# Kernel tuning notes

Measured on AMD Instinct MI355X. Metric: run time of the kernel, lower is better.

The kernel has to match this reference:

```python
import jax, jax.numpy as jnp
import numpy as np
import math

B, T, C = 2, 2048, 1024
H = 16
D = C // H


def setup_inputs() -> dict:
    key = jax.random.key(0)
    ks = jax.random.split(key, 5)
    s = 1.0 / math.sqrt(C)
    return {
        "x": jax.random.normal(ks[0], (B, T, C), dtype=jnp.float32),
        "W_qkv": jax.random.normal(ks[1], (C, 3 * C), dtype=jnp.float32) * s,
        "b_qkv": jnp.zeros((3 * C,), dtype=jnp.float32),
        "W_proj": jax.random.normal(ks[2], (C, C), dtype=jnp.float32) * s,
        "b_proj": jnp.zeros((C,), dtype=jnp.float32),
    }


def reference(x, W_qkv, b_qkv, W_proj, b_proj):
    qkv = x @ W_qkv + b_qkv  # [B,T,3C]
    q, k, v = jnp.split(qkv, 3, axis=-1)
    # [B,T,C] -> [B,H,T,D]
    q = q.reshape(B, T, H, D).transpose(0, 2, 1, 3)
    k = k.reshape(B, T, H, D).transpose(0, 2, 1, 3)
    v = v.reshape(B, T, H, D).transpose(0, 2, 1, 3)
    sm_scale = 1.0 / math.sqrt(D)
    att = jnp.einsum("bhqd,bhkd->bhqk", q, k) * sm_scale
    causal = jnp.tril(jnp.ones((T, T), dtype=bool))  # True = keep
    att = jnp.where(causal, att, -jnp.inf)
    att = jax.nn.softmax(att, axis=-1)
    y = jnp.einsum("bhqk,bhkd->bhqd", att, v)  # [B,H,T,D]
    y = y.transpose(0, 2, 1, 3).reshape(B, T, C)
    return y @ W_proj + b_proj
```

## Files before the change

kernel.cpp:

```cpp
#include <hip/hip_runtime.h>
#include <hip/hip_bf16.h>
#include <math.h>

#define BB 2
#define TT 2048
#define CCH 1024
#define HH 16
#define DD 64
#define BT (BB*TT)
#define N3 (3*CCH)
#define NJOBS 40

typedef __attribute__((ext_vector_type(8))) short short8;
typedef __attribute__((ext_vector_type(4))) float f32x4;
typedef __attribute__((ext_vector_type(16))) float f32x16;

__device__ __forceinline__ unsigned short f2bf(float f) {
  unsigned int u = __float_as_uint(f);
  unsigned int r = (u + 0x7FFFu + ((u >> 16) & 1u)) >> 16;
  return (unsigned short)r;
}
__device__ __forceinline__ float bf2f(unsigned short u) {
  return __uint_as_float(((unsigned int)u) << 16);
}
__device__ __forceinline__ int cvtpk(float lo, float hi) {
  int r;
  asm("v_cvt_pk_bf16_f32 %0, %1, %2" : "=v"(r) : "v"(lo), "v"(hi));
  return r;
}
__device__ __forceinline__ void plswap(int &a, int &b) {
  asm("v_permlane32_swap_b32 %0, %1" : "+v"(a), "+v"(b));
}
__device__ __forceinline__ float fexp2(float x) {
  float r;
  asm("v_exp_f32 %0, %1" : "=v"(r) : "v"(x));
  return r;
}
__device__ __forceinline__ void gload_lds16(const unsigned short* g, unsigned short* l) {
  __builtin_amdgcn_global_load_lds((const __attribute__((address_space(1))) void*)g,
                                   (__attribute__((address_space(3))) void*)l, 16, 0, 0);
}
__device__ __forceinline__ float fmax3(float a, float b, float c) {
  return fmaxf(fmaxf(a, b), c);
}
__device__ __forceinline__ int jbase(int qt) {
  int a = qt >> 2, b = qt & 3;
  return qt + 2 * a * (a - 1) + a * b;
}

__global__ __launch_bounds__(256) void k_convert(const float* __restrict__ in,
                                                 unsigned short* __restrict__ out, int n8) {
  int i = blockIdx.x * 256 + threadIdx.x;
  if (i < n8) {
    const float4 a = *(const float4*)(in + (size_t)i * 8);
    const float4 b = *(const float4*)(in + (size_t)i * 8 + 4);
    short8 v;
    v[0] = f2bf(a.x); v[1] = f2bf(a.y); v[2] = f2bf(a.z); v[3] = f2bf(a.w);
    v[4] = f2bf(b.x); v[5] = f2bf(b.y); v[6] = f2bf(b.z); v[7] = f2bf(b.w);
    *(short8*)(out + (size_t)i * 8) = v;
  }
}

__global__ __launch_bounds__(256) void k_transpose_cvt(const float* __restrict__ in,
                                                       unsigned short* __restrict__ out,
                                                       int R, int Cn) {
  __shared__ float tile[32][33];
  int tc = blockIdx.x * 32;
  int tr = blockIdx.y * 32;
  int lx = threadIdx.x & 31;
  int ly = threadIdx.x >> 5;
#pragma unroll
  for (int i = 0; i < 32; i += 8)
    tile[ly + i][lx] = in[(size_t)(tr + ly + i) * Cn + tc + lx];
  __syncthreads();
#pragma unroll
  for (int i = 0; i < 32; i += 8)
    out[(size_t)(tc + ly + i) * R + tr + lx] = f2bf(tile[lx][ly + i]);
}

__global__ __launch_bounds__(256) void k_qkv_gemm(const unsigned short* __restrict__ Xb,
                                                  const unsigned short* __restrict__ Wt,
                                                  const float* __restrict__ bias,
                                                  unsigned short* __restrict__ Qo,
                                                  unsigned short* __restrict__ Ko,
                                                  unsigned short* __restrict__ Vto) {
  __shared__ __align__(16) unsigned short As[128 * 32];
  __shared__ __align__(16) unsigned short Bs[128 * 32];
  int tid = threadIdx.x;
  int mb = blockIdx.x * 128;
  int nb = blockIdx.y * 128;
  int wid = tid >> 6, lane = tid & 63;
  int wr = (wid >> 1) * 64, wc = (wid & 1) * 64;
  int l15 = lane & 15, l4 = lane >> 4;
  int l16 = lane >> 2, lc = (lane & 3) * 8;
  f32x4 acc[4][4];
#pragma unroll
  for (int a = 0; a < 4; ++a)
#pragma unroll
    for (int b = 0; b < 4; ++b)
#pragma unroll
      for (int j = 0; j < 4; ++j) acc[a][b][j] = 0.0f;

  for (int kb = 0; kb < CCH; kb += 32) {
#pragma unroll
    for (int i = 0; i < 2; ++i) {
      int arow = wid * 32 + i * 16;
      gload_lds16(Xb + (size_t)(mb + arow + l16) * CCH + kb + lc, &As[arow * 32]);
      gload_lds16(Wt + (size_t)(nb + arow + l16) * CCH + kb + lc, &Bs[arow * 32]);
    }
    __syncthreads();
    short8 af[4], bfr[4];
#pragma unroll
    for (int mt = 0; mt < 4; ++mt) af[mt] = *(const short8*)(&As[(wr + mt * 16 + l15) * 32 + l4 * 8]);
#pragma unroll
    for (int nt = 0; nt < 4; ++nt) bfr[nt] = *(const short8*)(&Bs[(wc + nt * 16 + l15) * 32 + l4 * 8]);
#pragma unroll
    for (int mt = 0; mt < 4; ++mt)
#pragma unroll
      for (int nt = 0; nt < 4; ++nt)
        acc[mt][nt] = __builtin_amdgcn_mfma_f32_16x16x32_bf16(af[mt], bfr[nt], acc[mt][nt], 0, 0, 0);
    __syncthreads();
  }

#pragma unroll
  for (int mt = 0; mt < 4; ++mt) {
#pragma unroll
    for (int nt = 0; nt < 4; ++nt) {
      int gcol = nb + wc + nt * 16 + l15;
      int which = gcol >> 10;
      int cc = gcol & 1023;
      int h = cc >> 6, d = cc & 63;
      float bv = bias[gcol];
#pragma unroll
      for (int j = 0; j < 4; ++j) {
        int grow = mb + wr + mt * 16 + l4 * 4 + j;
        int b = grow >> 11, t = grow & 2047;
        float v = acc[mt][nt][j] + bv;
        size_t bh = (size_t)(b * HH + h);
        if (which == 0)      Qo[(bh * TT + t) * DD + d] = f2bf(v * 0.18033688f);
        else if (which == 1) Ko[(bh * TT + t) * DD + d] = f2bf(v);
        else                 Vto[(bh * DD + d) * TT + t] = f2bf(v);
      }
    }
  }
}

__global__ __launch_bounds__(256) void k_attn(const unsigned short* __restrict__ Qb,
                                              const unsigned short* __restrict__ Kb,
                                              const unsigned short* __restrict__ Vtb,
                                              unsigned short* __restrict__ PO,
                                              float* __restrict__ Pm,
                                              float* __restrict__ Pl) {
  __shared__ unsigned short Ks[2][64 * 64];
  __shared__ unsigned short Vs[2][64 * 64];
  int tid = threadIdx.x;
  int jx = blockIdx.x;
  int bh = blockIdx.y;
  int qt = 0;
#pragma unroll
  for (int q = 1; q < 16; ++q)
    if (jx >= jbase(q)) qt = q;
  int chunk = jx - jbase(qt);
  int t0 = chunk * 8;
  int t1 = min(t0 + 8, (qt + 1) * 2);
  size_t job = (size_t)bh * NJOBS + jx;

  const unsigned short* Qp = Qb + (size_t)bh * TT * DD;
  const unsigned short* Kp = Kb + (size_t)bh * TT * DD;
  const unsigned short* Vp = Vtb + (size_t)bh * DD * TT;
  int wid = tid >> 6, lane = tid & 63;
  int l31 = lane & 31, h = lane >> 5;
  int q0 = qt * 128 + wid * 32;
  int qrow = q0 + l31;

  short8 qf[4];
#pragma unroll
  for (int m = 0; m < 4; ++m)
    qf[m] = *(const short8*)(Qp + (size_t)qrow * DD + m * 16 + h * 8);

  f32x16 zv;
#pragma unroll
  for (int r = 0; r < 16; ++r) zv[r] = 0.0f;

  f32x16 po[2];
  po[0] = zv; po[1] = zv;
  float mrun = -1e30f, lrun = 0.0f;

  short8 rk[2], rv[2];
#pragma unroll
  for (int i = 0; i < 2; ++i) {
    int idx = tid + i * 256;
    int row = idx >> 3, c = idx & 7;
    rk[i] = *(const short8*)(Kp + (size_t)(t0 * 64 + row) * DD + c * 8);
    rv[i] = *(const short8*)(Vp + (size_t)row * TT + t0 * 64 + c * 8);
  }
#pragma unroll
  for (int i = 0; i < 2; ++i) {
    int idx = tid + i * 256;
    int row = idx >> 3, c = idx & 7;
    int off = row * 64 + ((c ^ (row & 7)) * 8);
    *(short8*)(&Ks[0][off]) = rk[i];
    *(short8*)(&Vs[0][off]) = rv[i];
  }

  int buf = 0;
  for (int t = t0; t < t1; ++t) {
    __syncthreads();
    int kvb = t * 64;
    bool havenext = (t + 1 < t1);
    if (havenext) {
      int kvb2 = (t + 1) * 64;
#pragma unroll
      for (int i = 0; i < 2; ++i) {
        int idx = tid + i * 256;
        int row = idx >> 3, c = idx & 7;
        rk[i] = *(const short8*)(Kp + (size_t)(kvb2 + row) * DD + c * 8);
        rv[i] = *(const short8*)(Vp + (size_t)row * TT + kvb2 + c * 8);
      }
    }

    if (kvb <= q0 + 31) {
      f32x16 st[2];
      __builtin_amdgcn_s_setprio(1);
#pragma unroll
      for (int t32 = 0; t32 < 2; ++t32) {
        int row = t32 * 32 + l31;
        {
          int off = row * 64 + ((h ^ (row & 7)) * 8);
          short8 kf = *(const short8*)(&Ks[buf][off]);
          st[t32] = __builtin_amdgcn_mfma_f32_32x32x16_bf16(kf, qf[0], zv, 0, 0, 0);
        }
#pragma unroll
        for (int m = 1; m < 4; ++m) {
          int off = row * 64 + (((2 * m + h) ^ (row & 7)) * 8);
          short8 kf = *(const short8*)(&Ks[buf][off]);
          st[t32] = __builtin_amdgcn_mfma_f32_32x32x16_bf16(kf, qf[m], st[t32], 0, 0, 0);
        }
      }
      __builtin_amdgcn_s_setprio(0);

      if (kvb + 63 > q0) {
#pragma unroll
        for (int t32 = 0; t32 < 2; ++t32)
#pragma unroll
          for (int r = 0; r < 16; ++r) {
            int kvg = kvb + t32 * 32 + (r & 3) + 8 * (r >> 2) + 4 * h;
            if (kvg > qrow) st[t32][r] = -1e30f;
          }
      }

      float A = st[0][0], B = st[0][1], C = st[0][2], Dv = st[0][3];
#pragma unroll
      for (int r = 4; r < 16; r += 4) {
        A = fmax3(A, st[0][r], st[0][r + 1]);
        B = fmax3(B, st[0][r + 2], st[0][r + 3]);
        C = fmax3(C, st[1][r - 4], st[1][r - 3]);
        Dv = fmax3(Dv, st[1][r - 2], st[1][r - 1]);
      }
      C = fmax3(C, st[1][12], st[1][13]);
      Dv = fmax3(Dv, st[1][14], st[1][15]);
      float mx = fmaxf(fmax3(A, B, C), Dv);
      mx = fmaxf(mx, __shfl_xor(mx, 32));

      if (__any(mx - mrun > 8.0f)) {
        float mnew = fmaxf(mrun, mx);
        float alpha = fexp2(mrun - mnew);
        lrun *= alpha;
#pragma unroll
        for (int dt = 0; dt < 2; ++dt)
#pragma unroll
          for (int r = 0; r < 16; ++r) po[dt][r] *= alpha;
        mrun = mnew;
      }

      float sum = 0.0f;
#pragma unroll
      for (int t32 = 0; t32 < 2; ++t32)
#pragma unroll
        for (int r = 0; r < 16; ++r) {
          float p = fexp2(st[t32][r] - mrun);
          st[t32][r] = p;
          sum += p;
        }
      sum += __shfl_xor(sum, 32);
      lrun += sum;

      short8 pf[4];
#pragma unroll
      for (int g = 0; g < 4; ++g) {
        int t32 = g >> 1, r0 = (g & 1) * 8;
        int a = cvtpk(st[t32][r0 + 0], st[t32][r0 + 1]);
        int b = cvtpk(st[t32][r0 + 4], st[t32][r0 + 5]);
        plswap(a, b);
        int c = cvtpk(st[t32][r0 + 2], st[t32][r0 + 3]);
        int d = cvtpk(st[t32][r0 + 6], st[t32][r0 + 7]);
        plswap(c, d);
        union { int w[4]; short8 s; } u;
        u.w[0] = a; u.w[1] = c; u.w[2] = b; u.w[3] = d;
        pf[g] = u.s;
      }

      __builtin_amdgcn_s_setprio(1);
#pragma unroll
      for (int dt = 0; dt < 2; ++dt) {
#pragma unroll
        for (int g = 0; g < 4; ++g) {
          int row = dt * 32 + l31;
          int off = row * 64 + (((2 * g + h) ^ (row & 7)) * 8);
          short8 vf = *(const short8*)(&Vs[buf][off]);
          po[dt] = __builtin_amdgcn_mfma_f32_32x32x16_bf16(vf, pf[g], po[dt], 0, 0, 0);
        }
      }
      __builtin_amdgcn_s_setprio(0);
    }

    if (havenext) {
#pragma unroll
      for (int i = 0; i < 2; ++i) {
        int idx = tid + i * 256;
        int row = idx >> 3, c = idx & 7;
        int off = row * 64 + ((c ^ (row & 7)) * 8);
        *(short8*)(&Ks[buf ^ 1][off]) = rk[i];
        *(short8*)(&Vs[buf ^ 1][off]) = rv[i];
      }
    }
    buf ^= 1;
  }

  int wrow = wid * 32 + l31;
  size_t pobase = (job * 128 + wrow) * 64;
#pragma unroll
  for (int dt = 0; dt < 2; ++dt)
#pragma unroll
    for (int r = 0; r < 16; r += 2) {
      int d = dt * 32 + (r & 3) + 8 * (r >> 2) + 4 * h;
      int w = cvtpk(po[dt][r], po[dt][r + 1]);
      *(int*)(PO + pobase + d) = w;
    }
  if (h == 0) {
    Pm[job * 128 + wrow] = mrun;
    Pl[job * 128 + wrow] = lrun;
  }
}

__global__ __launch_bounds__(256) void k_attn_combine(const unsigned short* __restrict__ PO,
                                                      const float* __restrict__ Pm,
                                                      const float* __restrict__ Pl,
                                                      unsigned short* __restrict__ Y) {
  int qt = blockIdx.x, bh = blockIdx.y;
  int nc = (qt >> 2) + 1;
  size_t job0 = (size_t)bh * NJOBS + jbase(qt);
  int tid = threadIdx.x;
  int row = tid >> 1, half = tid & 1;

  float m[4], l[4];
  float M = -1e30f;
  for (int c = 0; c < nc; ++c) {
    m[c] = Pm[(job0 + c) * 128 + row];
    l[c] = Pl[(job0 + c) * 128 + row];
    M = fmaxf(M, m[c]);
  }
  float L = 0.0f, w[4];
  for (int c = 0; c < nc; ++c) {
    w[c] = fexp2(m[c] - M);
    L += l[c] * w[c];
  }
  float inv = 1.0f / L;

  float acc[32];
#pragma unroll
  for (int j = 0; j < 32; ++j) acc[j] = 0.0f;
  for (int c = 0; c < nc; ++c) {
    const unsigned short* p = PO + ((job0 + c) * 128 + row) * 64 + half * 32;
    float wc = w[c];
#pragma unroll
    for (int k = 0; k < 4; ++k) {
      short8 v = *(const short8*)(p + k * 8);
#pragma unroll
      for (int j = 0; j < 8; ++j) acc[k * 8 + j] += wc * bf2f((unsigned short)v[j]);
    }
  }
  int b = bh >> 4, hh = bh & 15;
  int t = qt * 128 + row;
  unsigned short* yp = Y + ((size_t)(b * TT + t)) * CCH + hh * DD + half * 32;
#pragma unroll
  for (int k = 0; k < 4; ++k) {
    short8 wv;
#pragma unroll
    for (int j = 0; j < 8; ++j) wv[j] = (short)f2bf(acc[k * 8 + j] * inv);
    *(short8*)(yp + k * 8) = wv;
  }
}

__global__ __launch_bounds__(256) void k_proj_gemm(const unsigned short* __restrict__ Yb,
                                                   const unsigned short* __restrict__ Wt,
                                                   const float* __restrict__ bias,
                                                   float* __restrict__ Out) {
  __shared__ __align__(16) unsigned short As[128 * 32];
  __shared__ __align__(16) unsigned short Bs[128 * 32];
  int tid = threadIdx.x;
  int mb = blockIdx.x * 128;
  int nb = blockIdx.y * 128;
  int wid = tid >> 6, lane = tid & 63;
  int wr = (wid >> 1) * 64, wc = (wid & 1) * 64;
  int l15 = lane & 15, l4 = lane >> 4;
  int l16 = lane >> 2, lc = (lane & 3) * 8;
  f32x4 acc[4][4];
#pragma unroll
  for (int a = 0; a < 4; ++a)
#pragma unroll
    for (int b = 0; b < 4; ++b)
#pragma unroll
      for (int j = 0; j < 4; ++j) acc[a][b][j] = 0.0f;

  for (int kb = 0; kb < CCH; kb += 32) {
#pragma unroll
    for (int i = 0; i < 2; ++i) {
      int arow = wid * 32 + i * 16;
      gload_lds16(Yb + (size_t)(mb + arow + l16) * CCH + kb + lc, &As[arow * 32]);
      gload_lds16(Wt + (size_t)(nb + arow + l16) * CCH + kb + lc, &Bs[arow * 32]);
    }
    __syncthreads();
    short8 af[4], bfr[4];
#pragma unroll
    for (int mt = 0; mt < 4; ++mt) af[mt] = *(const short8*)(&As[(wr + mt * 16 + l15) * 32 + l4 * 8]);
#pragma unroll
    for (int nt = 0; nt < 4; ++nt) bfr[nt] = *(const short8*)(&Bs[(wc + nt * 16 + l15) * 32 + l4 * 8]);
#pragma unroll
    for (int mt = 0; mt < 4; ++mt)
#pragma unroll
      for (int nt = 0; nt < 4; ++nt)
        acc[mt][nt] = __builtin_amdgcn_mfma_f32_16x16x32_bf16(af[mt], bfr[nt], acc[mt][nt], 0, 0, 0);
    __syncthreads();
  }

#pragma unroll
  for (int mt = 0; mt < 4; ++mt) {
#pragma unroll
    for (int nt = 0; nt < 4; ++nt) {
      int gcol = nb + wc + nt * 16 + l15;
      float bv = bias[gcol];
#pragma unroll
      for (int j = 0; j < 4; ++j) {
        int grow = mb + wr + mt * 16 + l4 * 4 + j;
        Out[(size_t)grow * CCH + gcol] = acc[mt][nt][j] + bv;
      }
    }
  }
}

extern "C" void kernel_launch(void* const* d_in, const int* in_sizes, int n_in,
                              void* d_out, int out_size, void* d_ws, size_t ws_size,
                              hipStream_t stream) {
  const float* x      = (const float*)d_in[0];
  const float* W_qkv  = (const float*)d_in[1];
  const float* b_qkv  = (const float*)d_in[2];
  const float* W_proj = (const float*)d_in[3];
  const float* b_proj = (const float*)d_in[4];
  float* out = (float*)d_out;

  char* ws = (char*)d_ws;
  size_t off = 0;
  unsigned short* Wt_qkv  = (unsigned short*)(ws + off); off += (size_t)N3 * CCH * 2;
  unsigned short* Wt_proj = (unsigned short*)(ws + off); off += (size_t)CCH * CCH * 2;
  unsigned short* Xb      = (unsigned short*)(ws + off); off += (size_t)BT * CCH * 2;
  unsigned short* Qb      = (unsigned short*)(ws + off); off += (size_t)BT * CCH * 2;
  unsigned short* Kb      = (unsigned short*)(ws + off); off += (size_t)BT * CCH * 2;
  unsigned short* Vt      = (unsigned short*)(ws + off); off += (size_t)BT * CCH * 2;
  unsigned short* Yb      = (unsigned short*)(ws + off); off += (size_t)BT * CCH * 2;
  unsigned short* PO      = (unsigned short*)(ws + off); off += (size_t)32 * NJOBS * 128 * 64 * 2;
  float*          Pm      = (float*)(ws + off);          off += (size_t)32 * NJOBS * 128 * 4;
  float*          Pl      = (float*)(ws + off);          off += (size_t)32 * NJOBS * 128 * 4;

  k_convert<<<dim3(BT * CCH / 8 / 256), 256, 0, stream>>>(x, Xb, BT * CCH / 8);
  k_transpose_cvt<<<dim3(N3 / 32, CCH / 32), 256, 0, stream>>>(W_qkv, Wt_qkv, CCH, N3);
  k_transpose_cvt<<<dim3(CCH / 32, CCH / 32), 256, 0, stream>>>(W_proj, Wt_proj, CCH, CCH);
  k_qkv_gemm<<<dim3(BT / 128, N3 / 128), 256, 0, stream>>>(Xb, Wt_qkv, b_qkv, Qb, Kb, Vt);
  k_attn<<<dim3(NJOBS, BB * HH), 256, 0, stream>>>(Qb, Kb, Vt, PO, Pm, Pl);
  k_attn_combine<<<dim3(TT / 128, BB * HH), 256, 0, stream>>>(PO, Pm, Pl, Yb);
  k_proj_gemm<<<dim3(BT / 128, CCH / 128), 256, 0, stream>>>(Yb, Wt_proj, b_proj, out);
}
```

Baseline: 130.2 us.

## Read K/V fragments directly from global memory instead of LDS double buffer

Removes the shared-memory double-buffered K/V staging and the per-iteration barrier from the attention kernel. Each wave now loads its MFMA K and V operand fragments straight from global memory, relying on L1/L2 caching for reuse across the four waves, and exits the loop early once past the causal limit. This drops the LDS traffic and the sync, and frees LDS for higher occupancy. In exchange each wave issues redundant global loads with no explicit prefetch, so load latency lands directly on the MFMA chain.

```diff
diff --git a/kernel.cpp b/kernel.cpp
--- a/kernel.cpp
+++ b/kernel.cpp
@@ -151,8 +151,6 @@
                                               unsigned short* __restrict__ PO,
                                               float* __restrict__ Pm,
                                               float* __restrict__ Pl) {
-  __shared__ unsigned short Ks[2][64 * 64];
-  __shared__ unsigned short Vs[2][64 * 64];
   int tid = threadIdx.x;
   int jx = blockIdx.x;
   int bh = blockIdx.y;
@@ -186,145 +184,94 @@
   po[0] = zv; po[1] = zv;
   float mrun = -1e30f, lrun = 0.0f;
 
-  short8 rk[2], rv[2];
-#pragma unroll
-  for (int i = 0; i < 2; ++i) {
-    int idx = tid + i * 256;
-    int row = idx >> 3, c = idx & 7;
-    rk[i] = *(const short8*)(Kp + (size_t)(t0 * 64 + row) * DD + c * 8);
-    rv[i] = *(const short8*)(Vp + (size_t)row * TT + t0 * 64 + c * 8);
-  }
-#pragma unroll
-  for (int i = 0; i < 2; ++i) {
-    int idx = tid + i * 256;
-    int row = idx >> 3, c = idx & 7;
-    int off = row * 64 + ((c ^ (row & 7)) * 8);
-    *(short8*)(&Ks[0][off]) = rk[i];
-    *(short8*)(&Vs[0][off]) = rv[i];
-  }
-
-  int buf = 0;
   for (int t = t0; t < t1; ++t) {
-    __syncthreads();
     int kvb = t * 64;
-    bool havenext = (t + 1 < t1);
-    if (havenext) {
-      int kvb2 = (t + 1) * 64;
-#pragma unroll
-      for (int i = 0; i < 2; ++i) {
-        int idx = tid + i * 256;
-        int row = idx >> 3, c = idx & 7;
-        rk[i] = *(const short8*)(Kp + (size_t)(kvb2 + row) * DD + c * 8);
-        rv[i] = *(const short8*)(Vp + (size_t)row * TT + kvb2 + c * 8);
+    if (kvb > q0 + 31) break;
+
+    f32x16 st[2];
+    __builtin_amdgcn_s_setprio(1);
+#pragma unroll
+    for (int t32 = 0; t32 < 2; ++t32) {
+      const unsigned short* kbase = Kp + (size_t)(kvb + t32 * 32 + l31) * DD + h * 8;
+      st[t32] = __builtin_amdgcn_mfma_f32_32x32x16_bf16(*(const short8*)kbase, qf[0], zv, 0, 0, 0);
+#pragma unroll
+      for (int m = 1; m < 4; ++m)
+        st[t32] = __builtin_amdgcn_mfma_f32_32x32x16_bf16(*(const short8*)(kbase + m * 16), qf[m],
+                                                          st[t32], 0, 0, 0);
+    }
+    __builtin_amdgcn_s_setprio(0);
+
+    if (kvb + 63 > q0) {
+#pragma unroll
+      for (int t32 = 0; t32 < 2; ++t32)
+#pragma unroll
+        for (int r = 0; r < 16; ++r) {
+          int kvg = kvb + t32 * 32 + (r & 3) + 8 * (r >> 2) + 4 * h;
+          if (kvg > qrow) st[t32][r] = -1e30f;
+        }
+    }
+
+    float A = st[0][0], B = st[0][1], C = st[0][2], Dv = st[0][3];
+#pragma unroll
+    for (int r = 4; r < 16; r += 4) {
+      A = fmax3(A, st[0][r], st[0][r + 1]);
+      B = fmax3(B, st[0][r + 2], st[0][r + 3]);
+      C = fmax3(C, st[1][r - 4], st[1][r - 3]);
+      Dv = fmax3(Dv, st[1][r - 2], st[1][r - 1]);
+    }
+    C = fmax3(C, st[1][12], st[1][13]);
+    Dv = fmax3(Dv, st[1][14], st[1][15]);
+    float mx = fmaxf(fmax3(A, B, C), Dv);
+    mx = fmaxf(mx, __shfl_xor(mx, 32));
+
+    if (__any(mx - mrun > 8.0f)) {
+      float mnew = fmaxf(mrun, mx);
+      float alpha = fexp2(mrun - mnew);
+      lrun *= alpha;
+#pragma unroll
+      for (int dt = 0; dt < 2; ++dt)
+#pragma unroll
+        for (int r = 0; r < 16; ++r) po[dt][r] *= alpha;
+      mrun = mnew;
+    }
+
+    float sum = 0.0f;
+#pragma unroll
+    for (int t32 = 0; t32 < 2; ++t32)
+#pragma unroll
+      for (int r = 0; r < 16; ++r) {
+        float p = fexp2(st[t32][r] - mrun);
+        st[t32][r] = p;
+        sum += p;
       }
-    }
-
-    if (kvb <= q0 + 31) {
-      f32x16 st[2];
-      __builtin_amdgcn_s_setprio(1);
-#pragma unroll
-      for (int t32 = 0; t32 < 2; ++t32) {
-        int row = t32 * 32 + l31;
-        {
-          int off = row * 64 + ((h ^ (row & 7)) * 8);
-          short8 kf = *(const short8*)(&Ks[buf][off]);
-          st[t32] = __builtin_amdgcn_mfma_f32_32x32x16_bf16(kf, qf[0], zv, 0, 0, 0);
-        }
-#pragma unroll
-        for (int m = 1; m < 4; ++m) {
-          int off = row * 64 + (((2 * m + h) ^ (row & 7)) * 8);
-          short8 kf = *(const short8*)(&Ks[buf][off]);
-          st[t32] = __builtin_amdgcn_mfma_f32_32x32x16_bf16(kf, qf[m], st[t32], 0, 0, 0);
-        }
-      }
-      __builtin_amdgcn_s_setprio(0);
-
-      if (kvb + 63 > q0) {
-#pragma unroll
-        for (int t32 = 0; t32 < 2; ++t32)
-#pragma unroll
-          for (int r = 0; r < 16; ++r) {
-            int kvg = kvb + t32 * 32 + (r & 3) + 8 * (r >> 2) + 4 * h;
-            if (kvg > qrow) st[t32][r] = -1e30f;
-          }
-      }
-
-      float A = st[0][0], B = st[0][1], C = st[0][2], Dv = st[0][3];
-#pragma unroll
-      for (int r = 4; r < 16; r += 4) {
-        A = fmax3(A, st[0][r], st[0][r + 1]);
-        B = fmax3(B, st[0][r + 2], st[0][r + 3]);
-        C = fmax3(C, st[1][r - 4], st[1][r - 3]);
-        Dv = fmax3(Dv, st[1][r - 2], st[1][r - 1]);
-      }
-      C = fmax3(C, st[1][12], st[1][13]);
-      Dv = fmax3(Dv, st[1][14], st[1][15]);
-      float mx = fmaxf(fmax3(A, B, C), Dv);
-      mx = fmaxf(mx, __shfl_xor(mx, 32));
-
-      if (__any(mx - mrun > 8.0f)) {
-        float mnew = fmaxf(mrun, mx);
-        float alpha = fexp2(mrun - mnew);
-        lrun *= alpha;
-#pragma unroll
-        for (int dt = 0; dt < 2; ++dt)
-#pragma unroll
-          for (int r = 0; r < 16; ++r) po[dt][r] *= alpha;
-        mrun = mnew;
-      }
-
-      float sum = 0.0f;
-#pragma unroll
-      for (int t32 = 0; t32 < 2; ++t32)
-#pragma unroll
-        for (int r = 0; r < 16; ++r) {
-          float p = fexp2(st[t32][r] - mrun);
-          st[t32][r] = p;
-          sum += p;
-        }
-      sum += __shfl_xor(sum, 32);
-      lrun += sum;
-
-      short8 pf[4];
-#pragma unroll
-      for (int g = 0; g < 4; ++g) {
-        int t32 = g >> 1, r0 = (g & 1) * 8;
-        int a = cvtpk(st[t32][r0 + 0], st[t32][r0 + 1]);
-        int b = cvtpk(st[t32][r0 + 4], st[t32][r0 + 5]);
-        plswap(a, b);
-        int c = cvtpk(st[t32][r0 + 2], st[t32][r0 + 3]);
-        int d = cvtpk(st[t32][r0 + 6], st[t32][r0 + 7]);
-        plswap(c, d);
-        union { int w[4]; short8 s; } u;
-        u.w[0] = a; u.w[1] = c; u.w[2] = b; u.w[3] = d;
-        pf[g] = u.s;
-      }
-
-      __builtin_amdgcn_s_setprio(1);
-#pragma unroll
-      for (int dt = 0; dt < 2; ++dt) {
-#pragma unroll
-        for (int g = 0; g < 4; ++g) {
-          int row = dt * 32 + l31;
-          int off = row * 64 + (((2 * g + h) ^ (row & 7)) * 8);
-          short8 vf = *(const short8*)(&Vs[buf][off]);
-          po[dt] = __builtin_amdgcn_mfma_f32_32x32x16_bf16(vf, pf[g], po[dt], 0, 0, 0);
-        }
-      }
-      __builtin_amdgcn_s_setprio(0);
-    }
-
-    if (havenext) {
-#pragma unroll
-      for (int i = 0; i < 2; ++i) {
-        int idx = tid + i * 256;
-        int row = idx >> 3, c = idx & 7;
-        int off = row * 64 + ((c ^ (row & 7)) * 8);
-        *(short8*)(&Ks[buf ^ 1][off]) = rk[i];
-        *(short8*)(&Vs[buf ^ 1][off]) = rv[i];
-      }
-    }
-    buf ^= 1;
+    sum += __shfl_xor(sum, 32);
+    lrun += sum;
+
+    short8 pf[4];
+#pragma unroll
+    for (int g = 0; g < 4; ++g) {
+      int t32 = g >> 1, r0 = (g & 1) * 8;
+      int a = cvtpk(st[t32][r0 + 0], st[t32][r0 + 1]);
+      int b = cvtpk(st[t32][r0 + 4], st[t32][r0 + 5]);
+      plswap(a, b);
+      int c = cvtpk(st[t32][r0 + 2], st[t32][r0 + 3]);
+      int d = cvtpk(st[t32][r0 + 6], st[t32][r0 + 7]);
+      plswap(c, d);
+      union { int w[4]; short8 s; } u;
+      u.w[0] = a; u.w[1] = c; u.w[2] = b; u.w[3] = d;
+      pf[g] = u.s;
+    }
+
+    __builtin_amdgcn_s_setprio(1);
+#pragma unroll
+    for (int dt = 0; dt < 2; ++dt) {
+      const unsigned short* vbase = Vp + (size_t)(dt * 32 + l31) * TT + kvb + h * 8;
+#pragma unroll
+      for (int g = 0; g < 4; ++g)
+        po[dt] = __builtin_amdgcn_mfma_f32_32x32x16_bf16(*(const short8*)(vbase + g * 16), pf[g],
+                                                         po[dt], 0, 0, 0);
+    }
+    __builtin_amdgcn_s_setprio(0);
   }
 
   int wrow = wid * 32 + l31;
```

After: 176.5 us. 35.5% more time.
